# Kernel tuning notes

Hardware: AMD Instinct MI355X
Metric: run time of the kernel (lower is better)

The kernel has to match this reference:

```python
import jax, jax.numpy as jnp
import numpy as np


def setup_inputs() -> dict:
    key = jax.random.key(0)
    k1, k2 = jax.random.split(key)
    image_features = jax.random.normal(k1, (8192, 128), dtype=jnp.float32)
    gts = jax.random.normal(k2, (16384, 128), dtype=jnp.float32)
    return {"image_features": image_features, "gts": gts}


def reference(image_features, gts):
    # (same math as subtract-square-sum-sqrt, O(N*M) memory instead of O(N*M*D))
    x_sq = jnp.sum(image_features * image_features, axis=-1, keepdims=True)  # [N,1]
    g_sq = jnp.sum(gts * gts, axis=-1)[None, :]                              # [1,M]
    xg = jnp.einsum('nd,md->nm', image_features, gts)                        # [N,M]
    d2 = jnp.maximum(x_sq + g_sq - 2.0 * xg, 0.0)
    logits = -jnp.sqrt(d2)
    return logits
```

## Files before the change

### kernel.cpp

```cpp
#include <hip/hip_runtime.h>


#define N_IMG 8192
#define N_GTS 16384
#define K_DIM 128
#define BM 128
#define BN 128
#define LDS_K 64
#define LDAH 72

typedef __attribute__((ext_vector_type(8))) short short8;
typedef __attribute__((ext_vector_type(4))) float f32x4;

__device__ __forceinline__ unsigned short f2bf(float x) {
    unsigned int u = __float_as_uint(x);
    u += 0x7FFFu + ((u >> 16) & 1u);
    return (unsigned short)(u >> 16);
}

__global__ __launch_bounds__(256, 2)
void l2sim_kernel(const float* __restrict__ A, const float* __restrict__ G,
                  float* __restrict__ out)
{
    __shared__ short a_s[BM][LDAH];
    __shared__ short b_s[BN][LDAH];
    __shared__ float xsq_s[2][BM];
    __shared__ float gsq_s[2][BN];

    const int t  = threadIdx.x;
    const int bm = blockIdx.y;
    const int bn = blockIdx.x;

    const int wave = t >> 6;
    const int lane = t & 63;
    const int wm   = (wave & 1) << 6;
    const int wn   = (wave >> 1) << 6;
    const int lm   = lane & 15;
    const int quad = lane >> 4;

    f32x4 acc[4][4] = {};

    #pragma unroll
    for (int h = 0; h < 2; ++h) {
        if (h) __syncthreads();

        {
            const float* gA = A + (size_t)bm * BM * K_DIM + h * LDS_K;
            #pragma unroll
            for (int i = 0; i < 8; ++i) {
                int f   = i * 256 + t;
                int row = f >> 4;
                int c4  = f & 15;
                float4 v = *(const float4*)(gA + (size_t)row * K_DIM + c4 * 4);
                float s = v.x*v.x + v.y*v.y + v.z*v.z + v.w*v.w;
                s += __shfl_down(s, 8, 16);
                s += __shfl_down(s, 4, 16);
                s += __shfl_down(s, 2, 16);
                s += __shfl_down(s, 1, 16);
                short4 bv;
                bv.x = (short)f2bf(v.x);
                bv.y = (short)f2bf(v.y);
                bv.z = (short)f2bf(v.z);
                bv.w = (short)f2bf(v.w);
                *(short4*)&a_s[row][c4 * 4] = bv;
                if ((t & 15) == 0) xsq_s[h][row] = s;
            }
        }
        {
            const float* gB = G + (size_t)bn * BN * K_DIM + h * LDS_K;
            #pragma unroll
            for (int i = 0; i < 8; ++i) {
                int f   = i * 256 + t;
                int row = f >> 4;
                int c4  = f & 15;
                float4 v = *(const float4*)(gB + (size_t)row * K_DIM + c4 * 4);
                float s = v.x*v.x + v.y*v.y + v.z*v.z + v.w*v.w;
                s += __shfl_down(s, 8, 16);
                s += __shfl_down(s, 4, 16);
                s += __shfl_down(s, 2, 16);
                s += __shfl_down(s, 1, 16);
                short4 bv;
                bv.x = (short)f2bf(v.x);
                bv.y = (short)f2bf(v.y);
                bv.z = (short)f2bf(v.z);
                bv.w = (short)f2bf(v.w);
                *(short4*)&b_s[row][c4 * 4] = bv;
                if ((t & 15) == 0) gsq_s[h][row] = s;
            }
        }
        __syncthreads();

        #pragma unroll
        for (int ks = 0; ks < 2; ++ks) {
            short8 af[4], bfr[4];
            #pragma unroll
            for (int mi = 0; mi < 4; ++mi)
                af[mi] = *(const short8*)&a_s[wm + mi * 16 + lm][ks * 32 + quad * 8];
            #pragma unroll
            for (int ni = 0; ni < 4; ++ni)
                bfr[ni] = *(const short8*)&b_s[wn + ni * 16 + lm][ks * 32 + quad * 8];
            #pragma unroll
            for (int mi = 0; mi < 4; ++mi)
                #pragma unroll
                for (int ni = 0; ni < 4; ++ni)
                    acc[mi][ni] = __builtin_amdgcn_mfma_f32_16x16x32_bf16(
                        af[mi], bfr[ni], acc[mi][ni], 0, 0, 0);
        }
    }

    float* outBase = out + (size_t)bm * BM * N_GTS + (size_t)bn * BN;
    #pragma unroll
    for (int mi = 0; mi < 4; ++mi) {
        #pragma unroll
        for (int r = 0; r < 4; ++r) {
            int m_loc = wm + mi * 16 + quad * 4 + r;
            float xs = xsq_s[0][m_loc] + xsq_s[1][m_loc];
            float* orow = outBase + (size_t)m_loc * N_GTS;
            #pragma unroll
            for (int ni = 0; ni < 4; ++ni) {
                int n_loc = wn + ni * 16 + lm;
                float gs = gsq_s[0][n_loc] + gsq_s[1][n_loc];
                float d2 = fmaxf(xs + gs - 2.0f * acc[mi][ni][r], 0.0f);
                orow[n_loc] = -sqrtf(d2);
            }
        }
    }
}

extern "C" void kernel_launch(void* const* d_in, const int* in_sizes, int n_in,
                              void* d_out, int out_size, void* d_ws, size_t ws_size,
                              hipStream_t stream) {
    const float* A = (const float*)d_in[0];
    const float* G = (const float*)d_in[1];
    float* out = (float*)d_out;
    dim3 grid(N_GTS / BN, N_IMG / BM);
    l2sim_kernel<<<grid, 256, 0, stream>>>(A, G, out);
}
```

Before: 796.9 us.

## Stage epilogue through LDS for full-row vectorized output stores

Each wave now owns a 32-row by 128-column band instead of a 64x64 quadrant. After the MMA loop, the LDS tile buffers are reused through a union as per-wave scratch: finished logits are written there, then read back and stored to global memory as float4 writes that cover whole 512-byte rows. Before, each lane did scattered scalar stores in 64-byte segments. The aim is to make the very large output write coalesced, at the cost of an extra barrier and an LDS round-trip in the epilogue.

```diff
diff --git a/kernel.cpp b/kernel.cpp
--- a/kernel.cpp
+++ b/kernel.cpp
@@ -8,6 +8,7 @@
 #define BN 128
 #define LDS_K 64
 #define LDAH 72
+#define SCR_W 132
 
 typedef __attribute__((ext_vector_type(8))) short short8;
 typedef __attribute__((ext_vector_type(4))) float f32x4;
@@ -18,12 +19,16 @@
     return (unsigned short)(u >> 16);
 }
 
+union SMem {
+    struct { short a[BM][LDAH]; short b[BN][LDAH]; } t;
+    float scratch[4][16][SCR_W];
+};
+
 __global__ __launch_bounds__(256, 2)
 void l2sim_kernel(const float* __restrict__ A, const float* __restrict__ G,
                   float* __restrict__ out)
 {
-    __shared__ short a_s[BM][LDAH];
-    __shared__ short b_s[BN][LDAH];
+    __shared__ SMem sm;
     __shared__ float xsq_s[2][BM];
     __shared__ float gsq_s[2][BN];
 
@@ -33,12 +38,11 @@
 
     const int wave = t >> 6;
     const int lane = t & 63;
-    const int wm   = (wave & 1) << 6;
-    const int wn   = (wave >> 1) << 6;
     const int lm   = lane & 15;
     const int quad = lane >> 4;
+    const int band = wave * 32;
 
-    f32x4 acc[4][4] = {};
+    f32x4 acc[2][8] = {};
 
     #pragma unroll
     for (int h = 0; h < 2; ++h) {
@@ -48,9 +52,7 @@
             const float* gA = A + (size_t)bm * BM * K_DIM + h * LDS_K;
             #pragma unroll
             for (int i = 0; i < 8; ++i) {
-                int f   = i * 256 + t;
-                int row = f >> 4;
-                int c4  = f & 15;
+                int f = i * 256 + t, row = f >> 4, c4 = f & 15;
                 float4 v = *(const float4*)(gA + (size_t)row * K_DIM + c4 * 4);
                 float s = v.x*v.x + v.y*v.y + v.z*v.z + v.w*v.w;
                 s += __shfl_down(s, 8, 16);
@@ -58,11 +60,9 @@
                 s += __shfl_down(s, 2, 16);
                 s += __shfl_down(s, 1, 16);
                 short4 bv;
-                bv.x = (short)f2bf(v.x);
-                bv.y = (short)f2bf(v.y);
-                bv.z = (short)f2bf(v.z);
-                bv.w = (short)f2bf(v.w);
-                *(short4*)&a_s[row][c4 * 4] = bv;
+                bv.x = (short)f2bf(v.x); bv.y = (short)f2bf(v.y);
+                bv.z = (short)f2bf(v.z); bv.w = (short)f2bf(v.w);
+                *(short4*)&sm.t.a[row][c4 * 4] = bv;
                 if ((t & 15) == 0) xsq_s[h][row] = s;
             }
         }
@@ -70,9 +70,7 @@
             const float* gB = G + (size_t)bn * BN * K_DIM + h * LDS_K;
             #pragma unroll
             for (int i = 0; i < 8; ++i) {
-                int f   = i * 256 + t;
-                int row = f >> 4;
-                int c4  = f & 15;
+                int f = i * 256 + t, row = f >> 4, c4 = f & 15;
                 float4 v = *(const float4*)(gB + (size_t)row * K_DIM + c4 * 4);
                 float s = v.x*v.x + v.y*v.y + v.z*v.z + v.w*v.w;
                 s += __shfl_down(s, 8, 16);
@@ -80,11 +78,9 @@
                 s += __shfl_down(s, 2, 16);
                 s += __shfl_down(s, 1, 16);
                 short4 bv;
-                bv.x = (short)f2bf(v.x);
-                bv.y = (short)f2bf(v.y);
-                bv.z = (short)f2bf(v.z);
-                bv.w = (short)f2bf(v.w);
-                *(short4*)&b_s[row][c4 * 4] = bv;
+                bv.x = (short)f2bf(v.x); bv.y = (short)f2bf(v.y);
+                bv.z = (short)f2bf(v.z); bv.w = (short)f2bf(v.w);
+                *(short4*)&sm.t.b[row][c4 * 4] = bv;
                 if ((t & 15) == 0) gsq_s[h][row] = s;
             }
         }
@@ -92,37 +88,55 @@
 
         #pragma unroll
         for (int ks = 0; ks < 2; ++ks) {
-            short8 af[4], bfr[4];
+            short8 af[2], bfr[8];
             #pragma unroll
-            for (int mi = 0; mi < 4; ++mi)
-                af[mi] = *(const short8*)&a_s[wm + mi * 16 + lm][ks * 32 + quad * 8];
+            for (int mi = 0; mi < 2; ++mi)
+                af[mi] = *(const short8*)&sm.t.a[band + mi * 16 + lm][ks * 32 + quad * 8];
             #pragma unroll
-            for (int ni = 0; ni < 4; ++ni)
-                bfr[ni] = *(const short8*)&b_s[wn + ni * 16 + lm][ks * 32 + quad * 8];
+            for (int ni = 0; ni < 8; ++ni)
+                bfr[ni] = *(const short8*)&sm.t.b[ni * 16 + lm][ks * 32 + quad * 8];
             #pragma unroll
-            for (int mi = 0; mi < 4; ++mi)
+            for (int mi = 0; mi < 2; ++mi)
                 #pragma unroll
-                for (int ni = 0; ni < 4; ++ni)
+                for (int ni = 0; ni < 8; ++ni)
                     acc[mi][ni] = __builtin_amdgcn_mfma_f32_16x16x32_bf16(
                         af[mi], bfr[ni], acc[mi][ni], 0, 0, 0);
         }
     }
 
-    float* outBase = out + (size_t)bm * BM * N_GTS + (size_t)bn * BN;
+    float gs[8], xs[2][4];
     #pragma unroll
-    for (int mi = 0; mi < 4; ++mi) {
+    for (int ni = 0; ni < 8; ++ni) {
+        int n = ni * 16 + lm;
+        gs[ni] = gsq_s[0][n] + gsq_s[1][n];
+    }
+    #pragma unroll
+    for (int mi = 0; mi < 2; ++mi)
         #pragma unroll
         for (int r = 0; r < 4; ++r) {
-            int m_loc = wm + mi * 16 + quad * 4 + r;
-            float xs = xsq_s[0][m_loc] + xsq_s[1][m_loc];
-            float* orow = outBase + (size_t)m_loc * N_GTS;
+            int m = band + mi * 16 + quad * 4 + r;
+            xs[mi][r] = xsq_s[0][m] + xsq_s[1][m];
+        }
+
+    __syncthreads();
+
+    float* outBase = out + (size_t)(bm * BM) * N_GTS + (size_t)(bn * BN);
+    #pragma unroll
+    for (int mi = 0; mi < 2; ++mi) {
+        #pragma unroll
+        for (int ni = 0; ni < 8; ++ni)
             #pragma unroll
-            for (int ni = 0; ni < 4; ++ni) {
-                int n_loc = wn + ni * 16 + lm;
-                float gs = gsq_s[0][n_loc] + gsq_s[1][n_loc];
-                float d2 = fmaxf(xs + gs - 2.0f * acc[mi][ni][r], 0.0f);
-                orow[n_loc] = -sqrtf(d2);
+            for (int r = 0; r < 4; ++r) {
+                float d2 = fmaxf(xs[mi][r] + gs[ni] - 2.0f * acc[mi][ni][r], 0.0f);
+                sm.scratch[wave][quad * 4 + r][ni * 16 + lm] = -sqrtf(d2);
             }
+        #pragma unroll
+        for (int i = 0; i < 8; ++i) {
+            int r = i * 2 + (lane >> 5);
+            int c = (lane & 31) * 4;
+            f32x4 v = *(const f32x4*)&sm.scratch[wave][r][c];
+            int gr = band + mi * 16 + r;
+            *(f32x4*)(outBase + (size_t)gr * N_GTS + c) = v;
         }
     }
 }
```

After: 859.3 us. 1.08x slower.
